# Optimization experiments

Measured on AMD Instinct MI355X. Metric: run time of the kernel, lower is better.

The kernel has to match this reference:

```python
import jax, jax.numpy as jnp
import numpy as np

N_NODES = 100000
N_EDGES = 1600000
NODE_DIM = 128
EDGE_DIM = 32
HIDDEN_DIM = 256


def _linear_params(key, fan_in, fan_out):
    kw, kb = jax.random.split(key)
    bound = 1.0 / np.sqrt(fan_in)
    W = jax.random.uniform(kw, (fan_in, fan_out), minval=-bound, maxval=bound, dtype=jnp.float32)
    b = jax.random.uniform(kb, (fan_out,), minval=-bound, maxval=bound, dtype=jnp.float32)
    return W, b


def setup_inputs() -> dict:
    key = jax.random.key(0)
    ks = jax.random.split(key, 8)
    x = jax.random.normal(ks[0], (N_NODES, NODE_DIM), dtype=jnp.float32)
    edge_index = jax.random.randint(ks[1], (2, N_EDGES), 0, N_NODES, dtype=jnp.int64)
    edge_attr = jax.random.normal(ks[2], (N_EDGES, EDGE_DIM), dtype=jnp.float32)
    congestion = jax.random.uniform(ks[3], (N_NODES,), dtype=jnp.float32)
    msg_in = 2 * NODE_DIM + EDGE_DIM + 1
    mW1, mb1 = _linear_params(ks[4], msg_in, HIDDEN_DIM)
    mW2, mb2 = _linear_params(ks[5], HIDDEN_DIM, NODE_DIM)
    uW1, ub1 = _linear_params(ks[6], 2 * NODE_DIM, HIDDEN_DIM)
    uW2, ub2 = _linear_params(ks[7], HIDDEN_DIM, NODE_DIM)
    return {
        "x": x, "edge_index": edge_index, "edge_attr": edge_attr, "congestion": congestion,
        "mW1": mW1, "mb1": mb1, "mW2": mW2, "mb2": mb2,
        "uW1": uW1, "ub1": ub1, "uW2": uW2, "ub2": ub2,
    }


def reference(x, edge_index, edge_attr, congestion, mW1, mb1, mW2, mb2, uW1, ub1, uW2, ub2):
    src, dst = edge_index[0], edge_index[1]
    # gather node features and src congestion, concat along feature dim  [E, 2D+edge_dim+1]
    msg_in = jnp.concatenate(
        [x[src], x[dst], edge_attr, congestion[src][:, None]], axis=-1)
    h = jax.nn.relu(msg_in @ mW1 + mb1)          # [E, hidden]
    messages = h @ mW2 + mb2                     # [E, node_dim]
    # scatter_add messages into destination nodes  [N, node_dim]
    aggregated = jax.ops.segment_sum(messages, dst, num_segments=x.shape[0])
    upd_in = jnp.concatenate([x, aggregated], axis=-1)  # [N, 2*node_dim]
    h2 = jax.nn.relu(upd_in @ uW1 + ub1)
    x_new = h2 @ uW2 + ub2                       # [N, node_dim]
    return x_new
```

## Files before the change

kernel.cpp:

```cpp
#include <hip/hip_runtime.h>

#define E_TOTAL 1600000
#define NN 100000
#define D 128
#define ED 32
#define H 256

typedef __attribute__((ext_vector_type(8))) short s16x8;
typedef __attribute__((ext_vector_type(4))) short s16x4;
typedef __attribute__((ext_vector_type(4))) float f32x4;

#define MFMA(a, b, c) __builtin_amdgcn_mfma_f32_16x16x32_bf16((a), (b), (c), 0, 0, 0)

__device__ __forceinline__ short f2bf(float f) {
    unsigned u = __builtin_bit_cast(unsigned, f);
    u += 0x7fffu + ((u >> 16) & 1u);
    return (short)(u >> 16);
}
__device__ __forceinline__ float bf2f(short s) {
    return __builtin_bit_cast(float, ((unsigned)(unsigned short)s) << 16);
}

__device__ __forceinline__ void gll16(const void* g, void* l) {
    __builtin_amdgcn_global_load_lds(
        (const __attribute__((address_space(1))) void*)g,
        (__attribute__((address_space(3))) void*)l, 16, 0, 0);
}

__device__ __forceinline__ void swz_one(const float* __restrict__ W,
                                        short* __restrict__ out,
                                        int K, int N, int idx) {
    int j    = idx & 7;
    int lane = (idx >> 3) & 63;
    int rest = idx >> 9;
    int NT   = N >> 4;
    int nt   = rest % NT;
    int t    = rest / NT;
    int k    = t * 32 + (lane >> 4) * 8 + j;
    int col  = nt * 16 + (lane & 15);
    out[idx] = f2bf((k < K) ? W[k * N + col] : 0.f);
}

__global__ void k_prep(const float* __restrict__ x, short* __restrict__ xb,
                       const int* __restrict__ ei, int* __restrict__ cnt,
                       const float* __restrict__ mW1, short* __restrict__ W1s,
                       const float* __restrict__ mW2, short* __restrict__ W2s,
                       const float* __restrict__ uW1, short* __restrict__ U1s,
                       const float* __restrict__ uW2, short* __restrict__ U2s) {
    const int b = blockIdx.x;
    if (b < 12500) {
        int i = (b * 256 + threadIdx.x) * 4;
        if (i >= NN * D) return;
        f32x4 v = *(const f32x4*)(x + i);
        s16x4 o;
        o[0] = f2bf(v[0]); o[1] = f2bf(v[1]); o[2] = f2bf(v[2]); o[3] = f2bf(v[3]);
        *(s16x4*)(xb + i) = o;
    } else if (b < 18750) {
        int e = (b - 12500) * 256 + threadIdx.x;
        if (e < E_TOTAL) atomicAdd(&cnt[ei[E_TOTAL + e]], 1);
    } else {
        int idx = (b - 18750) * 256 + threadIdx.x;
        if (idx < 81920) { swz_one(mW1, W1s, 289, 256, idx); return; }
        idx -= 81920;
        if (idx < 32768) { swz_one(mW2, W2s, 256, 128, idx); return; }
        idx -= 32768;
        if (idx < 65536) { swz_one(uW1, U1s, 256, 256, idx); return; }
        idx -= 65536;
        if (idx < 32768) { swz_one(uW2, U2s, 256, 128, idx); }
    }
}

__global__ void k_scan1(int* __restrict__ cnt, int* __restrict__ psum, int n) {
    __shared__ int wsum[16];
    __shared__ int woff[16];
    const int tid = threadIdx.x, lane = tid & 63, wv = tid >> 6;
    int i = blockIdx.x * 1024 + tid;
    int v = (i < n) ? cnt[i] : 0;
    int s = v;
#pragma unroll
    for (int off = 1; off < 64; off <<= 1) {
        int u = __shfl_up(s, off, 64);
        if (lane >= off) s += u;
    }
    if (lane == 63) wsum[wv] = s;
    __syncthreads();
    if (wv == 0 && lane < 16) {
        int t = wsum[lane];
        int sc = t;
#pragma unroll
        for (int off = 1; off < 16; off <<= 1) {
            int u = __shfl_up(sc, off, 16);
            if (lane >= off) sc += u;
        }
        woff[lane] = sc - t;
    }
    __syncthreads();
    int excl = (s - v) + woff[wv];
    if (i < n) cnt[i] = excl;
    if (tid == 1023) psum[blockIdx.x] = excl + v;
}

__global__ void k_scan2(int* __restrict__ psum, int nb) {
    __shared__ int w0;
    const int tid = threadIdx.x, lane = tid & 63, wv = tid >> 6;
    int v = (tid < nb) ? psum[tid] : 0;
    int s = v;
#pragma unroll
    for (int off = 1; off < 64; off <<= 1) {
        int u = __shfl_up(s, off, 64);
        if (lane >= off) s += u;
    }
    if (wv == 0 && lane == 63) w0 = s;
    __syncthreads();
    int excl = (s - v) + (wv ? w0 : 0);
    if (tid < nb) psum[tid] = excl;
}

__global__ void k_scan3(const int* __restrict__ psum, int* __restrict__ cnt, int n) {
    int i = blockIdx.x * 1024 + threadIdx.x;
    if (i < n) cnt[i] += psum[blockIdx.x];
}

__global__ void k_perm(const int* __restrict__ ei, int* __restrict__ cursor,
                       int* __restrict__ perm, int2* __restrict__ srcdst) {
    int e = blockIdx.x * blockDim.x + threadIdx.x;
    if (e >= E_TOTAL) return;
    int s = ei[e], d = ei[E_TOTAL + e];
    int pos = atomicAdd(&cursor[d], 1);
    perm[pos] = e;
    srcdst[pos] = make_int2(s, d);
}

__global__ __launch_bounds__(512, 4)
void k_pre(const short* __restrict__ xb, const short* __restrict__ W1s,
           short* __restrict__ ys, short* __restrict__ yd) {
    __shared__ char smem[32768];
    const int tid  = threadIdx.x;
    const int lane = tid & 63;
    const int w    = tid >> 6;
    const int eh   = w >> 2;
    const int cg   = w & 3;
    const int m    = lane & 15;
    const int q    = lane >> 4;
    const int r0   = blockIdx.x * 128;

    {
        int rowl = w * 16 + (lane >> 2);
        int grow = r0 + rowl;
        int gc   = grow < NN ? grow : 0;
        int kqs  = (lane & 3) ^ ((lane >> 3) & 3);
        const char* gx = (const char*)xb + (long)gc * 256 + kqs * 16;
#pragma unroll
        for (int t = 0; t < 4; t++)
            gll16(gx + t * 64, smem + t * 8192 + w * 1024);
    }
    __syncthreads();

    const int rdoff = m * 64 + ((q ^ ((m >> 1) & 3)) << 4);

#pragma unroll
    for (int pass = 0; pass < 2; pass++) {
        f32x4 acc[4][4];
#pragma unroll
        for (int mt = 0; mt < 4; mt++)
#pragma unroll
            for (int n = 0; n < 4; n++) acc[mt][n] = (f32x4){0.f, 0.f, 0.f, 0.f};
#pragma unroll
        for (int t = 0; t < 4; t++) {
            s16x8 b[4];
            const short* bw = W1s + ((pass * 4 + t) * 16 + cg * 4) * 512 + lane * 8;
#pragma unroll
            for (int n = 0; n < 4; n++) b[n] = *(const s16x8*)(bw + n * 512);
#pragma unroll
            for (int mt = 0; mt < 4; mt++) {
                s16x8 a = *(const s16x8*)(smem + t * 8192 + (eh * 4 + mt) * 1024 + rdoff);
#pragma unroll
                for (int n = 0; n < 4; n++) acc[mt][n] = MFMA(a, b[n], acc[mt][n]);
            }
        }
        short* out = pass ? yd : ys;
#pragma unroll
        for (int mt = 0; mt < 4; mt++)
#pragma unroll
            for (int r = 0; r < 4; r++) {
                int grow = r0 + eh * 64 + mt * 16 + q * 4 + r;
                if (grow < NN) {
                    s16x4 o;
#pragma unroll
                    for (int n = 0; n < 4; n++) o[n] = f2bf(acc[mt][n][r]);
                    *(s16x4*)(out + (long)grow * 256 + (cg * 16 + m) * 4) = o;
                }
            }
    }
}

__global__ __launch_bounds__(512, 4)
void k_edge(const int* __restrict__ perm, const int2* __restrict__ srcdst,
            const short* __restrict__ ys, const short* __restrict__ yd,
            const float* __restrict__ eattr, const float* __restrict__ cong,
            const short* __restrict__ W1s, const float* __restrict__ b1,
            const short* __restrict__ W2s, const float* __restrict__ b2,
            float* __restrict__ agg) {
    __shared__ char smem[73728];
    __shared__ int   dst_s[128];
    __shared__ int   src_s[128];
    __shared__ short cong_s[128];

    const int tid  = threadIdx.x;
    const int lane = tid & 63;
    const int w    = tid >> 6;
    const int eh   = w >> 2;
    const int cg   = w & 3;
    const int m    = lane & 15;
    const int q    = lane >> 4;
    const int p0b  = blockIdx.x * 128;

    {
        int edge = w * 16 + (lane >> 2);
        int kqs  = (lane & 3) ^ ((lane >> 3) & 3);
        int ea = perm[p0b + edge];
        const float* ge = eattr + (long)ea * ED + kqs * 8;
        f32x4 e0 = *(const f32x4*)ge, e1 = *(const f32x4*)(ge + 4);
        s16x8 ev;
#pragma unroll
        for (int j = 0; j < 4; j++) { ev[j] = f2bf(e0[j]); ev[4 + j] = f2bf(e1[j]); }
        *(s16x8*)(smem + w * 1024 + lane * 16) = ev;
        if (tid < 128) {
            int2 sd2 = srcdst[p0b + tid];
            dst_s[tid]  = sd2.y;
            src_s[tid]  = sd2.x;
            cong_s[tid] = f2bf(cong[sd2.x]);
        }
    }
    __syncthreads();

    const int rdoff = m * 64 + ((q ^ ((m >> 1) & 3)) << 4);

    f32x4 acc[4][4];
#pragma unroll
    for (int mt = 0; mt < 4; mt++)
#pragma unroll
        for (int n = 0; n < 4; n++) acc[mt][n] = (f32x4){0.f, 0.f, 0.f, 0.f};

    {
        s16x8 b[4];
        const short* bw = W1s + (8 * 16 + cg * 4) * 512 + lane * 8;
#pragma unroll
        for (int n = 0; n < 4; n++) b[n] = *(const s16x8*)(bw + n * 512);
#pragma unroll
        for (int mt = 0; mt < 4; mt++) {
            s16x8 a = *(const s16x8*)(smem + (eh * 4 + mt) * 1024 + rdoff);
#pragma unroll
            for (int n = 0; n < 4; n++) acc[mt][n] = MFMA(a, b[n], acc[mt][n]);
        }
    }
    {
        s16x8 b[4];
        const short* bw = W1s + (9 * 16 + cg * 4) * 512 + lane * 8;
#pragma unroll
        for (int n = 0; n < 4; n++) b[n] = *(const s16x8*)(bw + n * 512);
#pragma unroll
        for (int mt = 0; mt < 4; mt++) {
            s16x8 a = (s16x8){0, 0, 0, 0, 0, 0, 0, 0};
            short cv = cong_s[eh * 64 + mt * 16 + m];
            a[0] = (q == 0) ? cv : (short)0;
#pragma unroll
            for (int n = 0; n < 4; n++) acc[mt][n] = MFMA(a, b[n], acc[mt][n]);
        }
    }

    {
        short* hb16 = (short*)(smem + 8192);
        float b1c[4];
#pragma unroll
        for (int n = 0; n < 4; n++) b1c[n] = b1[cg * 64 + n * 16 + m];
        const int qoff = (cg * 16 + m) * 4;
#pragma unroll
        for (int mt = 0; mt < 4; mt++) {
            s16x4 ysv[4], ydv[4];
#pragma unroll
            for (int r = 0; r < 4; r++) {
                int e = eh * 64 + mt * 16 + q * 4 + r;
                ysv[r] = *(const s16x4*)(ys + (long)src_s[e] * 256 + qoff);
                ydv[r] = *(const s16x4*)(yd + (long)dst_s[e] * 256 + qoff);
            }
#pragma unroll
            for (int r = 0; r < 4; r++) {
                int e = eh * 64 + mt * 16 + q * 4 + r;
                int key = (2 * q + (r >> 1)) & 3;
#pragma unroll
                for (int n = 0; n < 4; n++) {
                    const int chunk = 2 * cg + (n >> 1);
                    const int srq   = (n & 1) * 2 + (m >> 3);
                    int phys = srq ^ key;
                    float v = acc[mt][n][r] + b1c[n]
                            + bf2f(ysv[r][n]) + bf2f(ydv[r][n]);
                    hb16[chunk * 4096 + e * 32 + phys * 8 + (m & 7)] =
                        f2bf(v > 0.f ? v : 0.f);
                }
            }
        }
    }
    __syncthreads();

    f32x4 acc2[4][2];
#pragma unroll
    for (int mt = 0; mt < 4; mt++) {
        acc2[mt][0] = (f32x4){0.f, 0.f, 0.f, 0.f};
        acc2[mt][1] = (f32x4){0.f, 0.f, 0.f, 0.f};
    }
#pragma unroll
    for (int t2 = 0; t2 < 8; t2++) {
        const short* bw = W2s + (t2 * 8 + cg * 2) * 512 + lane * 8;
        s16x8 b0  = *(const s16x8*)bw;
        s16x8 b1v = *(const s16x8*)(bw + 512);
#pragma unroll
        for (int mt = 0; mt < 4; mt++) {
            s16x8 a = *(const s16x8*)(smem + 8192 + t2 * 8192
                                      + (eh * 4 + mt) * 1024 + rdoff);
            acc2[mt][0] = MFMA(a, b0, acc2[mt][0]);
            acc2[mt][1] = MFMA(a, b1v, acc2[mt][1]);
        }
    }
    __syncthreads();

    {
        float (*mbuf)[132] = (float (*)[132])smem;
        float bb0 = b2[cg * 32 + m];
        float bb1 = b2[cg * 32 + 16 + m];
#pragma unroll
        for (int mt = 0; mt < 4; mt++)
#pragma unroll
            for (int r = 0; r < 4; r++) {
                int edge = eh * 64 + mt * 16 + q * 4 + r;
                mbuf[edge][cg * 32 + m]      = acc2[mt][0][r] + bb0;
                mbuf[edge][cg * 32 + 16 + m] = acc2[mt][1][r] + bb1;
            }
    }
    __syncthreads();

    {
        float (*mbuf)[132] = (float (*)[132])smem;
        const int qtr = tid >> 7, cc = tid & 127;
        float s = 0.f;
        int prev = dst_s[qtr * 32];
        for (int row = qtr * 32; row < qtr * 32 + 32; row++) {
            int dcur = dst_s[row];
            if (dcur != prev) {
                __hip_atomic_fetch_add(agg + (long)prev * D + cc, s,
                                       __ATOMIC_RELAXED, __HIP_MEMORY_SCOPE_AGENT);
                s = 0.f; prev = dcur;
            }
            s += mbuf[row][cc];
        }
        __hip_atomic_fetch_add(agg + (long)prev * D + cc, s,
                               __ATOMIC_RELAXED, __HIP_MEMORY_SCOPE_AGENT);
    }
}

__global__ __launch_bounds__(512, 4)
void k_node(const short* __restrict__ xb, const float* __restrict__ agg,
            const short* __restrict__ U1s, const float* __restrict__ b1,
            const short* __restrict__ U2s, const float* __restrict__ b2,
            float* __restrict__ out) {
    __shared__ char smem[65536];
    const int tid  = threadIdx.x;
    const int lane = tid & 63;
    const int w    = tid >> 6;
    const int eh   = w >> 2;
    const int cg   = w & 3;
    const int m    = lane & 15;
    const int q    = lane >> 4;
    const int r0   = blockIdx.x * 128;

    {
        int rowl = w * 16 + (lane >> 2);
        int grow = r0 + rowl;
        int gc   = grow < NN ? grow : 0;
        int kqs  = (lane & 3) ^ ((lane >> 3) & 3);
        const char* gx = (const char*)xb + (long)gc * 256 + kqs * 16;
#pragma unroll
        for (int t = 0; t < 4; t++)
            gll16(gx + t * 64, smem + t * 8192 + w * 1024);
        const float* ga = agg + (long)gc * D + kqs * 8;
#pragma unroll
        for (int t = 0; t < 4; t++) {
            f32x4 a0 = *(const f32x4*)(ga + t * 32);
            f32x4 a1 = *(const f32x4*)(ga + t * 32 + 4);
            s16x8 v;
#pragma unroll
            for (int j = 0; j < 4; j++) { v[j] = f2bf(a0[j]); v[4 + j] = f2bf(a1[j]); }
            *(s16x8*)(smem + (4 + t) * 8192 + w * 1024 + lane * 16) = v;
        }
    }
    __syncthreads();

    const int rdoff = m * 64 + ((q ^ ((m >> 1) & 3)) << 4);

    f32x4 acc[4][4];
#pragma unroll
    for (int mt = 0; mt < 4; mt++)
#pragma unroll
        for (int n = 0; n < 4; n++) acc[mt][n] = (f32x4){0.f, 0.f, 0.f, 0.f};

#pragma unroll
    for (int t = 0; t < 8; t++) {
        s16x8 b[4];
        const short* bw = U1s + (t * 16 + cg * 4) * 512 + lane * 8;
#pragma unroll
        for (int n = 0; n < 4; n++) b[n] = *(const s16x8*)(bw + n * 512);
#pragma unroll
        for (int mt = 0; mt < 4; mt++) {
            s16x8 a = *(const s16x8*)(smem + t * 8192 + (eh * 4 + mt) * 1024 + rdoff);
#pragma unroll
            for (int n = 0; n < 4; n++) acc[mt][n] = MFMA(a, b[n], acc[mt][n]);
        }
    }
    __syncthreads();

    {
        short* hb16 = (short*)smem;
#pragma unroll
        for (int n = 0; n < 4; n++) {
            const int chunk = 2 * cg + (n >> 1);
            const int srq   = (n & 1) * 2 + (m >> 3);
            const float bias = b1[cg * 64 + n * 16 + m];
#pragma unroll
            for (int mt = 0; mt < 4; mt++) {
#pragma unroll
                for (int r = 0; r < 4; r++) {
                    int row = eh * 64 + mt * 16 + q * 4 + r;
                    int key = (2 * q + (r >> 1)) & 3;
                    int phys = srq ^ key;
                    float v = acc[mt][n][r] + bias;
                    hb16[chunk * 4096 + row * 32 + phys * 8 + (m & 7)] =
                        f2bf(v > 0.f ? v : 0.f);
                }
            }
        }
    }
    __syncthreads();

    f32x4 acc2[4][2];
#pragma unroll
    for (int mt = 0; mt < 4; mt++) {
        acc2[mt][0] = (f32x4){0.f, 0.f, 0.f, 0.f};
        acc2[mt][1] = (f32x4){0.f, 0.f, 0.f, 0.f};
    }
#pragma unroll
    for (int t2 = 0; t2 < 8; t2++) {
        const short* bw = U2s + (t2 * 8 + cg * 2) * 512 + lane * 8;
        s16x8 b0  = *(const s16x8*)bw;
        s16x8 b1v = *(const s16x8*)(bw + 512);
#pragma unroll
        for (int mt = 0; mt < 4; mt++) {
            s16x8 a = *(const s16x8*)(smem + t2 * 8192 + (eh * 4 + mt) * 1024 + rdoff);
            acc2[mt][0] = MFMA(a, b0, acc2[mt][0]);
            acc2[mt][1] = MFMA(a, b1v, acc2[mt][1]);
        }
    }

    {
        float bb0 = b2[cg * 32 + m];
        float bb1 = b2[cg * 32 + 16 + m];
#pragma unroll
        for (int mt = 0; mt < 4; mt++)
#pragma unroll
            for (int r = 0; r < 4; r++) {
                int grow = r0 + eh * 64 + mt * 16 + q * 4 + r;
                if (grow < NN) {
                    out[(long)grow * D + cg * 32 + m]      = acc2[mt][0][r] + bb0;
                    out[(long)grow * D + cg * 32 + 16 + m] = acc2[mt][1][r] + bb1;
                }
            }
    }
}

extern "C" void kernel_launch(void* const* d_in, const int* in_sizes, int n_in,
                              void* d_out, int out_size, void* d_ws, size_t ws_size,
                              hipStream_t stream) {
    const float* x     = (const float*)d_in[0];
    const int*   ei    = (const int*)d_in[1];
    const float* eattr = (const float*)d_in[2];
    const float* cong  = (const float*)d_in[3];
    const float* mW1   = (const float*)d_in[4];
    const float* mb1   = (const float*)d_in[5];
    const float* mW2   = (const float*)d_in[6];
    const float* mb2   = (const float*)d_in[7];
    const float* uW1   = (const float*)d_in[8];
    const float* ub1   = (const float*)d_in[9];
    const float* uW2   = (const float*)d_in[10];
    const float* ub2   = (const float*)d_in[11];

    char* ws = (char*)d_ws;
    float* agg    = (float*)ws;
    short* xb     = (short*)(ws + 51200000);
    short* W1s    = (short*)(ws + 76800000);
    short* W2s    = (short*)(ws + 76963840);
    short* U1s    = (short*)(ws + 77029376);
    short* U2s    = (short*)(ws + 77160448);
    int*   cnt    = (int*)(ws + 77225984);
    int*   perm   = (int*)(ws + 77625984);
    int2*  srcdst = (int2*)(ws + 84025984);
    int*   psum   = (int*)(ws + 96825984);
    short* yd     = (short*)(ws + 96826496);
    short* ys     = (short*)(ws + 148026496);

    hipMemsetAsync(agg, 0, (size_t)NN * D * sizeof(float), stream);
    hipMemsetAsync(cnt, 0, (size_t)NN * sizeof(int), stream);

    k_prep<<<19582, 256, 0, stream>>>(x, xb, ei, cnt,
                                      mW1, W1s, mW2, W2s, uW1, U1s, uW2, U2s);

    k_pre<<<(NN + 127) / 128, 512, 0, stream>>>(xb, W1s, ys, yd);

    int nb = (NN + 1023) / 1024;
    k_scan1<<<nb, 1024, 0, stream>>>(cnt, psum, NN);
    k_scan2<<<1, 128, 0, stream>>>(psum, nb);
    k_scan3<<<nb, 1024, 0, stream>>>(psum, cnt, NN);
    k_perm<<<(E_TOTAL + 255) / 256, 256, 0, stream>>>(ei, cnt, perm, srcdst);

    k_edge<<<E_TOTAL / 128, 512, 0, stream>>>(perm, srcdst, ys, yd, eattr, cong,
                                              W1s, mb1, W2s, mb2, agg);
    k_node<<<(NN + 127) / 128, 512, 0, stream>>>(xb, agg, U1s, ub1, U2s, ub2,
                                                 (float*)d_out);
}
```

Before: 925.3 us.

## Fold biases into precompute and agg init, chained single-pass scan

Replaces the three-kernel prefix scan with one decoupled-lookback scan kernel that chains block totals through a flag array. The b1 bias moves into the per-node precompute (ys), and the b2 bias is applied once per node as degree*b2 when agg is initialised, instead of per edge. This drops the large agg memset and per-edge bias adds in the edge kernel. The lookback relies on blocks being scheduled in order and adds an extra init kernel.

```diff
diff --git a/kernel.cpp b/kernel.cpp
--- a/kernel.cpp
+++ b/kernel.cpp
@@ -70,9 +70,11 @@
     }
 }
 
-__global__ void k_scan1(int* __restrict__ cnt, int* __restrict__ psum, int n) {
+__global__ void k_scanc(int* __restrict__ cnt, unsigned long long* __restrict__ chain,
+                        int n) {
     __shared__ int wsum[16];
     __shared__ int woff[16];
+    __shared__ int carry_s;
     const int tid = threadIdx.x, lane = tid & 63, wv = tid >> 6;
     int i = blockIdx.x * 1024 + tid;
     int v = (i < n) ? cnt[i] : 0;
@@ -96,29 +98,42 @@
     }
     __syncthreads();
     int excl = (s - v) + woff[wv];
-    if (i < n) cnt[i] = excl;
-    if (tid == 1023) psum[blockIdx.x] = excl + v;
-}
-
-__global__ void k_scan2(int* __restrict__ psum, int nb) {
-    __shared__ int w0;
-    const int tid = threadIdx.x, lane = tid & 63, wv = tid >> 6;
-    int v = (tid < nb) ? psum[tid] : 0;
-    int s = v;
-#pragma unroll
-    for (int off = 1; off < 64; off <<= 1) {
-        int u = __shfl_up(s, off, 64);
-        if (lane >= off) s += u;
-    }
-    if (wv == 0 && lane == 63) w0 = s;
-    __syncthreads();
-    int excl = (s - v) + (wv ? w0 : 0);
-    if (tid < nb) psum[tid] = excl;
-}
-
-__global__ void k_scan3(const int* __restrict__ psum, int* __restrict__ cnt, int n) {
-    int i = blockIdx.x * 1024 + threadIdx.x;
-    if (i < n) cnt[i] += psum[blockIdx.x];
+    if (tid == 1023) {
+        int btot = excl + v;
+        __hip_atomic_store(&chain[blockIdx.x], (1ull << 32) | (unsigned)btot,
+                           __ATOMIC_RELAXED, __HIP_MEMORY_SCOPE_AGENT);
+        int pfx = 0;
+        for (int j = (int)blockIdx.x - 1; j >= 0; --j) {
+            unsigned long long e;
+            do {
+                e = __hip_atomic_load(&chain[j], __ATOMIC_RELAXED,
+                                      __HIP_MEMORY_SCOPE_AGENT);
+            } while ((e >> 32) == 0);
+            pfx += (int)(unsigned)e;
+            if ((e >> 32) == 2) break;
+        }
+        __hip_atomic_store(&chain[blockIdx.x], (2ull << 32) | (unsigned)(pfx + btot),
+                           __ATOMIC_RELAXED, __HIP_MEMORY_SCOPE_AGENT);
+        carry_s = pfx;
+    }
+    __syncthreads();
+    if (i < n) cnt[i] = excl + carry_s;
+}
+
+__global__ void k_agginit(const int* __restrict__ cnt, const float* __restrict__ b2,
+                          float* __restrict__ agg) {
+    int i4 = (blockIdx.x * 256 + threadIdx.x) * 4;
+    if (i4 >= NN * D) return;
+    int node  = i4 >> 7;
+    int c     = i4 & 127;
+    int start = cnt[node];
+    int end   = (node < NN - 1) ? cnt[node + 1] : E_TOTAL;
+    float deg = (float)(end - start);
+    f32x4 bv = *(const f32x4*)(b2 + c);
+    f32x4 o;
+#pragma unroll
+    for (int j = 0; j < 4; j++) o[j] = deg * bv[j];
+    *(f32x4*)(agg + i4) = o;
 }
 
 __global__ void k_perm(const int* __restrict__ ei, int* __restrict__ cursor,
@@ -133,7 +148,8 @@
 
 __global__ __launch_bounds__(512, 4)
 void k_pre(const short* __restrict__ xb, const short* __restrict__ W1s,
-           short* __restrict__ ys, short* __restrict__ yd) {
+           const float* __restrict__ b1, short* __restrict__ ys,
+           short* __restrict__ yd) {
     __shared__ char smem[32768];
     const int tid  = threadIdx.x;
     const int lane = tid & 63;
@@ -158,6 +174,10 @@
 
     const int rdoff = m * 64 + ((q ^ ((m >> 1) & 3)) << 4);
 
+    float b1c[4];
+#pragma unroll
+    for (int n = 0; n < 4; n++) b1c[n] = b1[cg * 64 + n * 16 + m];
+
 #pragma unroll
     for (int pass = 0; pass < 2; pass++) {
         f32x4 acc[4][4];
@@ -187,7 +207,8 @@
                 if (grow < NN) {
                     s16x4 o;
 #pragma unroll
-                    for (int n = 0; n < 4; n++) o[n] = f2bf(acc[mt][n][r]);
+                    for (int n = 0; n < 4; n++)
+                        o[n] = f2bf(acc[mt][n][r] + (pass ? 0.f : b1c[n]));
                     *(s16x4*)(out + (long)grow * 256 + (cg * 16 + m) * 4) = o;
                 }
             }
@@ -198,8 +219,7 @@
 void k_edge(const int* __restrict__ perm, const int2* __restrict__ srcdst,
             const short* __restrict__ ys, const short* __restrict__ yd,
             const float* __restrict__ eattr, const float* __restrict__ cong,
-            const short* __restrict__ W1s, const float* __restrict__ b1,
-            const short* __restrict__ W2s, const float* __restrict__ b2,
+            const short* __restrict__ W1s, const short* __restrict__ W2s,
             float* __restrict__ agg) {
     __shared__ char smem[73728];
     __shared__ int   dst_s[128];
@@ -271,9 +291,6 @@
 
     {
         short* hb16 = (short*)(smem + 8192);
-        float b1c[4];
-#pragma unroll
-        for (int n = 0; n < 4; n++) b1c[n] = b1[cg * 64 + n * 16 + m];
         const int qoff = (cg * 16 + m) * 4;
 #pragma unroll
         for (int mt = 0; mt < 4; mt++) {
@@ -293,8 +310,7 @@
                     const int chunk = 2 * cg + (n >> 1);
                     const int srq   = (n & 1) * 2 + (m >> 3);
                     int phys = srq ^ key;
-                    float v = acc[mt][n][r] + b1c[n]
-                            + bf2f(ysv[r][n]) + bf2f(ydv[r][n]);
+                    float v = acc[mt][n][r] + bf2f(ysv[r][n]) + bf2f(ydv[r][n]);
                     hb16[chunk * 4096 + e * 32 + phys * 8 + (m & 7)] =
                         f2bf(v > 0.f ? v : 0.f);
                 }
@@ -326,15 +342,13 @@
 
     {
         float (*mbuf)[132] = (float (*)[132])smem;
-        float bb0 = b2[cg * 32 + m];
-        float bb1 = b2[cg * 32 + 16 + m];
 #pragma unroll
         for (int mt = 0; mt < 4; mt++)
 #pragma unroll
             for (int r = 0; r < 4; r++) {
                 int edge = eh * 64 + mt * 16 + q * 4 + r;
-                mbuf[edge][cg * 32 + m]      = acc2[mt][0][r] + bb0;
-                mbuf[edge][cg * 32 + 16 + m] = acc2[mt][1][r] + bb1;
+                mbuf[edge][cg * 32 + m]      = acc2[mt][0][r];
+                mbuf[edge][cg * 32 + 16 + m] = acc2[mt][1][r];
             }
     }
     __syncthreads();
@@ -500,28 +514,28 @@
     short* U1s    = (short*)(ws + 77029376);
     short* U2s    = (short*)(ws + 77160448);
     int*   cnt    = (int*)(ws + 77225984);
-    int*   perm   = (int*)(ws + 77625984);
-    int2*  srcdst = (int2*)(ws + 84025984);
-    int*   psum   = (int*)(ws + 96825984);
-    short* yd     = (short*)(ws + 96826496);
-    short* ys     = (short*)(ws + 148026496);
-
-    hipMemsetAsync(agg, 0, (size_t)NN * D * sizeof(float), stream);
-    hipMemsetAsync(cnt, 0, (size_t)NN * sizeof(int), stream);
+    unsigned long long* chain = (unsigned long long*)(ws + 77625984);
+    int*   perm   = (int*)(ws + 77627008);
+    int2*  srcdst = (int2*)(ws + 84027008);
+    short* yd     = (short*)(ws + 96827008);
+    short* ys     = (short*)(ws + 148027008);
+
+    hipMemsetAsync(cnt, 0, 401024, stream);
 
     k_prep<<<19582, 256, 0, stream>>>(x, xb, ei, cnt,
                                       mW1, W1s, mW2, W2s, uW1, U1s, uW2, U2s);
 
-    k_pre<<<(NN + 127) / 128, 512, 0, stream>>>(xb, W1s, ys, yd);
+    k_pre<<<(NN + 127) / 128, 512, 0, stream>>>(xb, W1s, mb1, ys, yd);
 
     int nb = (NN + 1023) / 1024;
-    k_scan1<<<nb, 1024, 0, stream>>>(cnt, psum, NN);
-    k_scan2<<<1, 128, 0, stream>>>(psum, nb);
-    k_scan3<<<nb, 1024, 0, stream>>>(psum, cnt, NN);
+    k_scanc<<<nb, 1024, 0, stream>>>(cnt, chain, NN);
+
+    k_agginit<<<12500, 256, 0, stream>>>(cnt, mb2, agg);
+
     k_perm<<<(E_TOTAL + 255) / 256, 256, 0, stream>>>(ei, cnt, perm, srcdst);
 
     k_edge<<<E_TOTAL / 128, 512, 0, stream>>>(perm, srcdst, ys, yd, eattr, cong,
-                                              W1s, mb1, W2s, mb2, agg);
+                                              W1s, W2s, agg);
     k_node<<<(NN + 127) / 128, 512, 0, stream>>>(xb, agg, U1s, ub1, U2s, ub2,
                                                  (float*)d_out);
 }
```

New measurement: 922.3 us. Within noise of the previous version (-0.3%).
